# Optimization experiments

Measured on AMD Instinct MI355X. Metric: run time of the kernel, lower is better.

The kernel has to match this reference:

```python
import jax, jax.numpy as jnp
import numpy as np

BATCH = 262144
WIN = 5
VOCAB = 100000
EMB = 50
HID = 250
OUT = 36


def setup_inputs() -> dict:
    key = jax.random.key(0)
    k1, k2, k3, k4, k5, k6 = jax.random.split(key, 6)
    idx = jax.random.randint(k1, (BATCH, WIN), 0, VOCAB, dtype=jnp.int64 if jax.config.jax_enable_x64 else jnp.int32)
    emb_table = jax.random.normal(k2, (VOCAB, EMB), dtype=jnp.float32) * 0.1
    w_in = jax.random.normal(k3, (WIN * EMB, HID), dtype=jnp.float32) * (1.0 / np.sqrt(WIN * EMB))
    b_in = jax.random.normal(k4, (HID,), dtype=jnp.float32) * 0.01
    w_out = jax.random.normal(k5, (HID, OUT), dtype=jnp.float32) * (1.0 / np.sqrt(HID))
    b_out = jax.random.normal(k6, (OUT,), dtype=jnp.float32) * 0.01
    return {"idx": idx, "emb_table": emb_table, "w_in": w_in, "b_in": b_in, "w_out": w_out, "b_out": b_out}


def reference(idx, emb_table, w_in, b_in, w_out, b_out):
    # Gather window embeddings; indices that are -1 or >= vocab map to zero vectors
    vocab = emb_table.shape[0]
    valid = (idx >= 0) & (idx < vocab)                       # [B, W]
    safe = jnp.clip(idx, 0, vocab - 1)
    emb = emb_table[safe] * valid[..., None].astype(emb_table.dtype)  # [B, W, E]
    x = emb.reshape(emb.shape[0], -1)                        # [B, W*E] concat
    h = jnp.tanh(x @ w_in + b_in)                            # [B, HID]
    return h @ w_out + b_out                                 # [B, OUT]
```

## Files before the change

### kernel.cpp

```cpp
#include <hip/hip_runtime.h>
#include <hip/hip_bf16.h>

#define TPB 256
#define PREP_TPB 256

constexpr int B_    = 262144;
constexpr int WIN_  = 5;
constexpr int VOCAB_= 100000;
constexpr int EMB_  = 50;
constexpr int HID_  = 250;
constexpr int OUT_  = 36;
constexpr int KP    = 256;
constexpr int NP    = 256;
constexpr int OP    = 48;
constexpr int BM    = 64;
constexpr int K1    = 320;
constexpr int ROWB  = 640;

typedef __attribute__((ext_vector_type(8))) short fragA;
typedef __attribute__((ext_vector_type(4))) float fragC;

__device__ __forceinline__ short f2b(float f) {
    __hip_bfloat16 h = __float2bfloat16(f);
    return *reinterpret_cast<short*>(&h);
}

__device__ __forceinline__ unsigned pack2(float x, float y) {
    return (unsigned)(unsigned short)f2b(x) | ((unsigned)(unsigned short)f2b(y) << 16);
}

__device__ __forceinline__ float fast_tanh(float x) {
    float e = __expf(2.f * x);
    return 1.f - __fdividef(2.f, e + 1.f);
}

__device__ __forceinline__ void* xp(char* xs, int row, int b) {
    return xs + row * ROWB + (b ^ ((row & 7) << 4));
}

__global__ void prep_emb(const float* __restrict__ emb, short* __restrict__ emb_b) {
    int id = blockIdx.x * PREP_TPB + threadIdx.x;
    if (id >= VOCAB_ * 32) return;
    int row = id >> 5, c2 = id & 31;
    unsigned v = 0u;
    if (c2 < 25) {
        float2 f = *(const float2*)(emb + row * EMB_ + 2 * c2);
        v = pack2(f.x, f.y);
    }
    ((unsigned*)emb_b)[id] = v;
}

__global__ void prep_weights(const float* __restrict__ w_in,
                             const float* __restrict__ w_out,
                             const float* __restrict__ b_in,
                             const float* __restrict__ b_out,
                             short* __restrict__ wT,
                             short* __restrict__ woT,
                             float* __restrict__ b_in_p,
                             float* __restrict__ b_out_p) {
    int id = blockIdx.x * PREP_TPB + threadIdx.x;
    if (id < 10 * NP * 32) {
        int kk = id / (NP * 32), r = id - kk * NP * 32;
        int n = r >> 5, j = r & 31;
        int k1 = kk * 32 + j;
        int w = k1 >> 6, e = k1 & 63;
        float v = (n < HID_ && e < EMB_) ? w_in[(w * EMB_ + e) * HID_ + n] : 0.f;
        wT[id] = f2b(v);
        return;
    }
    int id2 = id - 10 * NP * 32;
    if (id2 < 8 * OP * 32) {
        int kk = id2 / (OP * 32), r = id2 - kk * OP * 32;
        int o = r >> 5, j = r & 31;
        int k = kk * 32 + j;
        float v = (o < OUT_ && k < HID_) ? w_out[k * OUT_ + o] : 0.f;
        woT[id2] = f2b(v);
        return;
    }
    int id3 = id2 - 8 * OP * 32;
    if (id3 < NP) { b_in_p[id3] = (id3 < HID_) ? b_in[id3] : 0.f; return; }
    int id4 = id3 - NP;
    if (id4 < OP) { b_out_p[id4] = (id4 < OUT_) ? b_out[id4] : 0.f; }
}

template<bool BF>
__launch_bounds__(TPB, 4)
__global__ void tagger_main(const int* __restrict__ idx,
                            const float* __restrict__ emb,
                            const short* __restrict__ emb_b,
                            const float* __restrict__ b_in_p,
                            const float* __restrict__ b_out_p,
                            const short* __restrict__ wT,
                            const short* __restrict__ woT,
                            float* __restrict__ out) {
    __shared__ char xs[BM * ROWB];

    const int tid   = threadIdx.x;
    const int lane  = tid & 63;
    const int wave  = tid >> 6;
    const int l16   = lane & 15;
    const int khalf = lane >> 4;
    const int r0    = blockIdx.x * BM;

    if constexpr (BF) {
        #pragma unroll
        for (int it = 0; it < 10; ++it) {
            int c   = it * TPB + tid;
            int p   = c >> 3, sub = c & 7;
            int row = p / 5, win = p - row * 5;
            int iv  = idx[r0 * WIN_ + p];
            fragA v = {0, 0, 0, 0, 0, 0, 0, 0};
            if (iv >= 0 && iv < VOCAB_)
                v = *(const fragA*)(emb_b + iv * 64 + sub * 8);
            *(fragA*)xp(xs, row, win * 128 + sub * 16) = v;
        }
    } else {
        const int sub = tid & 3;
        #pragma unroll
        for (int it = 0; it < 5; ++it) {
            int p = it * 64 + (tid >> 2);
            int row = p / 5, win = p - row * 5;
            int iv  = idx[r0 * WIN_ + p];
            bool valid = (iv >= 0 && iv < VOCAB_);
            const float* base = emb + (valid ? iv : 0) * EMB_;
            #pragma unroll
            for (int j = 0; j < 7; ++j) {
                int ch = sub + 4 * j;
                if (ch < 25) {
                    float2 v = make_float2(0.f, 0.f);
                    if (valid) v = *(const float2*)(base + 2 * ch);
                    *(unsigned*)xp(xs, row, win * 128 + 4 * ch) = pack2(v.x, v.y);
                }
            }
            for (int ch = 25 + sub; ch < 32; ch += 4)
                *(unsigned*)xp(xs, row, win * 128 + 4 * ch) = 0u;
        }
    }
    __syncthreads();

    fragC acc[4][4];
    #pragma unroll
    for (int mf = 0; mf < 4; ++mf)
        #pragma unroll
        for (int nf = 0; nf < 4; ++nf)
            acc[mf][nf] = (fragC){0.f, 0.f, 0.f, 0.f};

    const int nb = wave * 64;
    const short* wbase = wT + (nb + l16) * 32 + khalf * 8;

    #pragma unroll 2
    for (int kk = 0; kk < 10; ++kk) {
        fragA a[4], b[4];
        #pragma unroll
        for (int mf = 0; mf < 4; ++mf)
            a[mf] = *(const fragA*)xp(xs, mf * 16 + l16, kk * 64 + khalf * 16);
        #pragma unroll
        for (int nf = 0; nf < 4; ++nf)
            b[nf] = *(const fragA*)(wbase + kk * (NP * 32) + nf * (16 * 32));
        #pragma unroll
        for (int mf = 0; mf < 4; ++mf)
            #pragma unroll
            for (int nf = 0; nf < 4; ++nf)
                acc[mf][nf] = __builtin_amdgcn_mfma_f32_16x16x32_bf16(b[nf], a[mf], acc[mf][nf], 0, 0, 0);
    }

    __syncthreads();

    #pragma unroll
    for (int nf = 0; nf < 4; ++nf) {
        const int n0 = nb + nf * 16 + khalf * 4;
        const float4 bi = *(const float4*)&b_in_p[n0];
        #pragma unroll
        for (int mf = 0; mf < 4; ++mf) {
            const int row = mf * 16 + l16;
            uint2 v;
            v.x = pack2(fast_tanh(acc[mf][nf][0] + bi.x), fast_tanh(acc[mf][nf][1] + bi.y));
            v.y = pack2(fast_tanh(acc[mf][nf][2] + bi.z), fast_tanh(acc[mf][nf][3] + bi.w));
            *(uint2*)xp(xs, row, 2 * n0) = v;
        }
    }
    __syncthreads();

    fragC acc2[3];
    #pragma unroll
    for (int of = 0; of < 3; ++of) acc2[of] = (fragC){0.f, 0.f, 0.f, 0.f};

    const short* wobase = woT + l16 * 32 + khalf * 8;

    #pragma unroll 2
    for (int kk = 0; kk < 8; ++kk) {
        fragA ha = *(const fragA*)xp(xs, wave * 16 + l16, 64 * kk + 16 * khalf);
        #pragma unroll
        for (int of = 0; of < 3; ++of) {
            fragA wb = *(const fragA*)(wobase + kk * (OP * 32) + of * (16 * 32));
            acc2[of] = __builtin_amdgcn_mfma_f32_16x16x32_bf16(wb, ha, acc2[of], 0, 0, 0);
        }
    }

    {
        const int row = r0 + wave * 16 + l16;
        #pragma unroll
        for (int of = 0; of < 3; ++of) {
            const int o0 = of * 16 + khalf * 4;
            if (o0 < OUT_) {
                const float4 bo = *(const float4*)&b_out_p[o0];
                float4 v;
                v.x = acc2[of][0] + bo.x;
                v.y = acc2[of][1] + bo.y;
                v.z = acc2[of][2] + bo.z;
                v.w = acc2[of][3] + bo.w;
                *(float4*)&out[row * OUT_ + o0] = v;
            }
        }
    }
}

extern "C" void kernel_launch(void* const* d_in, const int* in_sizes, int n_in,
                              void* d_out, int out_size, void* d_ws, size_t ws_size,
                              hipStream_t stream) {
    const int*   idx   = (const int*)d_in[0];
    const float* emb   = (const float*)d_in[1];
    const float* w_in  = (const float*)d_in[2];
    const float* b_in  = (const float*)d_in[3];
    const float* w_out = (const float*)d_in[4];
    const float* b_out = (const float*)d_in[5];
    float* out = (float*)d_out;

    const size_t emb_b_elems = (size_t)VOCAB_ * 64;
    const size_t tail_elems  = (size_t)10 * NP * 32 + 8 * OP * 32 + 2 * (NP + OP);
    const size_t need_bf = (emb_b_elems + tail_elems + 256) * 2;
    const bool bf = (ws_size >= need_bf);

    short* emb_b = nullptr;
    short* wT;
    if (bf) {
        emb_b = (short*)d_ws;
        wT    = emb_b + emb_b_elems;
        prep_emb<<<VOCAB_ * 32 / PREP_TPB, PREP_TPB, 0, stream>>>(emb, emb_b);
    } else {
        wT = (short*)d_ws;
    }
    short* woT = wT + 10 * NP * 32;
    float* b_in_p  = (float*)(woT + 8 * OP * 32);
    float* b_out_p = b_in_p + NP;

    int prep_threads = 10 * NP * 32 + 8 * OP * 32 + NP + OP;
    prep_weights<<<(prep_threads + PREP_TPB - 1) / PREP_TPB, PREP_TPB, 0, stream>>>(
        w_in, w_out, b_in, b_out, wT, woT, b_in_p, b_out_p);

    if (bf)
        tagger_main<true><<<B_ / BM, TPB, 0, stream>>>(idx, emb, emb_b, b_in_p, b_out_p, wT, woT, out);
    else
        tagger_main<false><<<B_ / BM, TPB, 0, stream>>>(idx, emb, emb_b, b_in_p, b_out_p, wT, woT, out);
}
```

Baseline: 99.62 us.

## Gather embeddings via direct global-to-LDS loads and fold tanh scaling into bias

The bf16 embedding gather now uses global_load_lds to copy rows straight into shared memory, skipping the register round trip. Invalid indices are redirected to an extra all-zero row appended to the bf16 table, so no branch is needed. Each thread's source address is computed from the swizzled LDS layout. The tanh is rewritten with exp2 and a hardware reciprocal, with the 2*log2(e) factor pre-folded into the bias, saving a multiply per element at some cost in accuracy.

```diff
diff --git a/kernel.cpp b/kernel.cpp
--- a/kernel.cpp
+++ b/kernel.cpp
@@ -17,6 +17,8 @@
 constexpr int K1    = 320;
 constexpr int ROWB  = 640;
 
+constexpr float TWO_LOG2E = 2.8853900817779268f;
+
 typedef __attribute__((ext_vector_type(8))) short fragA;
 typedef __attribute__((ext_vector_type(4))) float fragC;
 
@@ -29,9 +31,9 @@
     return (unsigned)(unsigned short)f2b(x) | ((unsigned)(unsigned short)f2b(y) << 16);
 }
 
-__device__ __forceinline__ float fast_tanh(float x) {
-    float e = __expf(2.f * x);
-    return 1.f - __fdividef(2.f, e + 1.f);
+__device__ __forceinline__ float tanh_b(float a, float b2) {
+    float e = __builtin_amdgcn_exp2f(__builtin_fmaf(a, TWO_LOG2E, b2));
+    return __builtin_fmaf(-2.f, __builtin_amdgcn_rcpf(e + 1.f), 1.f);
 }
 
 __device__ __forceinline__ void* xp(char* xs, int row, int b) {
@@ -40,10 +42,10 @@
 
 __global__ void prep_emb(const float* __restrict__ emb, short* __restrict__ emb_b) {
     int id = blockIdx.x * PREP_TPB + threadIdx.x;
-    if (id >= VOCAB_ * 32) return;
+    if (id >= (VOCAB_ + 1) * 32) return;
     int row = id >> 5, c2 = id & 31;
     unsigned v = 0u;
-    if (c2 < 25) {
+    if (row < VOCAB_ && c2 < 25) {
         float2 f = *(const float2*)(emb + row * EMB_ + 2 * c2);
         v = pack2(f.x, f.y);
     }
@@ -78,7 +80,7 @@
         return;
     }
     int id3 = id2 - 8 * OP * 32;
-    if (id3 < NP) { b_in_p[id3] = (id3 < HID_) ? b_in[id3] : 0.f; return; }
+    if (id3 < NP) { b_in_p[id3] = (id3 < HID_) ? b_in[id3] * TWO_LOG2E : 0.f; return; }
     int id4 = id3 - NP;
     if (id4 < OP) { b_out_p[id4] = (id4 < OUT_) ? b_out[id4] : 0.f; }
 }
@@ -105,14 +107,18 @@
     if constexpr (BF) {
         #pragma unroll
         for (int it = 0; it < 10; ++it) {
-            int c   = it * TPB + tid;
-            int p   = c >> 3, sub = c & 7;
-            int row = p / 5, win = p - row * 5;
-            int iv  = idx[r0 * WIN_ + p];
-            fragA v = {0, 0, 0, 0, 0, 0, 0, 0};
-            if (iv >= 0 && iv < VOCAB_)
-                v = *(const fragA*)(emb_b + iv * 64 + sub * 8);
-            *(fragA*)xp(xs, row, win * 128 + sub * 16) = v;
+            int o    = (it * TPB + tid) * 16;
+            int row  = o / ROWB;
+            int bs   = o - row * ROWB;
+            int win  = bs >> 7;
+            int boff = (bs & 127) ^ ((row & 7) << 4);
+            int iv   = idx[(r0 + row) * WIN_ + win];
+            unsigned safe = ((unsigned)iv < (unsigned)VOCAB_) ? (unsigned)iv : (unsigned)VOCAB_;
+            const short* src = emb_b + (size_t)safe * 64 + (boff >> 1);
+            __builtin_amdgcn_global_load_lds(
+                (const __attribute__((address_space(1))) unsigned int*)src,
+                (__attribute__((address_space(3))) unsigned int*)(xs + it * (TPB * 16) + wave * 1024),
+                16, 0, 0);
         }
     } else {
         const int sub = tid & 3;
@@ -174,8 +180,8 @@
         for (int mf = 0; mf < 4; ++mf) {
             const int row = mf * 16 + l16;
             uint2 v;
-            v.x = pack2(fast_tanh(acc[mf][nf][0] + bi.x), fast_tanh(acc[mf][nf][1] + bi.y));
-            v.y = pack2(fast_tanh(acc[mf][nf][2] + bi.z), fast_tanh(acc[mf][nf][3] + bi.w));
+            v.x = pack2(tanh_b(acc[mf][nf][0], bi.x), tanh_b(acc[mf][nf][1], bi.y));
+            v.y = pack2(tanh_b(acc[mf][nf][2], bi.z), tanh_b(acc[mf][nf][3], bi.w));
             *(uint2*)xp(xs, row, 2 * n0) = v;
         }
     }
@@ -226,7 +232,7 @@
     const float* b_out = (const float*)d_in[5];
     float* out = (float*)d_out;
 
-    const size_t emb_b_elems = (size_t)VOCAB_ * 64;
+    const size_t emb_b_elems = (size_t)(VOCAB_ + 1) * 64;
     const size_t tail_elems  = (size_t)10 * NP * 32 + 8 * OP * 32 + 2 * (NP + OP);
     const size_t need_bf = (emb_b_elems + tail_elems + 256) * 2;
     const bool bf = (ws_size >= need_bf);
@@ -236,7 +242,7 @@
     if (bf) {
         emb_b = (short*)d_ws;
         wT    = emb_b + emb_b_elems;
-        prep_emb<<<VOCAB_ * 32 / PREP_TPB, PREP_TPB, 0, stream>>>(emb, emb_b);
+        prep_emb<<<((VOCAB_ + 1) * 32 + PREP_TPB - 1) / PREP_TPB, PREP_TPB, 0, stream>>>(emb, emb_b);
     } else {
         wT = (short*)d_ws;
     }
```

Result: faster. 91.98 us (-7.7%).
